# Performance work log

Measured on AMD Instinct MI355X. Metric: run time of the kernel, lower is better.

Reference implementation:

```python
import jax, jax.numpy as jnp
import numpy as np
from jax.scipy.special import gammaln

D_CAT = 20000   # input_dim: number of multinomial categories (tree leaves)
HID = 128       # hidden_dim
BATCH = 128     # batch_size (must match eta's leading dim)
INIT = 1e-3     # init_scale
LOG_SIGMA_SQ0 = 0.01


def _balance_basis(D):
    """Sparse ILR balance basis (D-1, D) from a balanced binary tree.
    Row for an internal node with l left / r right leaves has
    +sqrt(r/(l(l+r))) on left leaves and -sqrt(l/(r(l+r))) on right leaves.
    Mirrors sparse_balance_basis(random_linkage(D)) structurally (rows sum to 0,
    orthonormal), with ~D*log2(D) nonzeros."""
    rows, cols, vals = [], [], []
    stack = [(0, D)]
    r = 0
    while stack:
        lo, hi = stack.pop()
        n = hi - lo
        if n < 2:
            continue
        mid = lo + n // 2
        l, rt = mid - lo, hi - mid
        a = np.sqrt(rt / (l * (l + rt)))
        b = -np.sqrt(l / (rt * (l + rt)))
        cols.extend(range(lo, hi))
        vals.extend([a] * l + [b] * rt)
        rows.extend([r] * n)
        r += 1
        stack.append((lo, mid))
        stack.append((mid, hi))
    assert r == D - 1
    return (np.asarray(rows, np.int32), np.asarray(cols, np.int32),
            np.asarray(vals, np.float32))


def setup_inputs() -> dict:
    key = jax.random.key(0)
    ks = jax.random.split(key, 4)
    rows, cols, vals = _balance_basis(D_CAT)
    x = jax.random.randint(ks[0], (BATCH, D_CAT), 0, 20).astype(jnp.float32)
    enc_w = jax.random.normal(ks[1], (HID, D_CAT - 1), jnp.float32) * INIT   # nn.Linear weight (out,in)
    dec_w = jax.random.normal(ks[2], (D_CAT - 1, HID), jnp.float32) * INIT
    eta = jax.random.normal(ks[3], (BATCH, D_CAT - 1), jnp.float32) * INIT
    return {
        "x": x,
        "psi_rows": jnp.asarray(rows),
        "psi_cols": jnp.asarray(cols),
        "psi_vals": jnp.asarray(vals),
        "enc_w": enc_w,
        "dec_w": dec_w,
        "variational_logvars": jnp.zeros((HID,), jnp.float32),
        "log_sigma_sq": jnp.float32(LOG_SIGMA_SQ0),
        "eta": eta,
    }


def reference(x, psi_rows, psi_cols, psi_vals, enc_w, dec_w,
              variational_logvars, log_sigma_sq, eta):
    B, D = x.shape
    dm1 = D - 1
    k = enc_w.shape[0]

    # ilr(imputer(x), Psi): hx = (Psi @ log(x+1)^T)^T via sparse gather+segment_sum
    lx = jnp.log(x + 1.0)                                  # (B, D)
    contrib = lx[:, psi_cols] * psi_vals                   # (B, nnz)
    hx = jax.ops.segment_sum(contrib.T, psi_rows, num_segments=dm1,
                             indices_are_sorted=True).T    # (B, D-1)

    z_mean = hx @ enc_w.T                                  # (B, k)
    mu = z_mean @ dec_w.T                                  # (B, D-1)

    # prior: standard Normal log-prob of z_mean, mean over all elements
    prior_loss = jnp.mean(-0.5 * z_mean ** 2 - 0.5 * jnp.log(2.0 * jnp.pi))

    # MultivariateNormalFactorIdentity(mu, var, Dv, W): Sigma = var*I + W diag(Dv) W^T
    # Woodbury / matrix-determinant-lemma log-prob of eta.
    var = jnp.exp(log_sigma_sq)
    Dv = jnp.exp(variational_logvars)                      # (k,)
    sD = jnp.sqrt(Dv)
    WtW = dec_w.T @ dec_w                                  # (k, k)
    M = jnp.eye(k, dtype=x.dtype) + (sD[:, None] * WtW * sD[None, :]) / var
    _, logdetM = jnp.linalg.slogdet(M)
    logdet = dm1 * log_sigma_sq + logdetM                  # log|Sigma|
    diff = eta - mu                                        # (B, D-1)
    u = (diff @ dec_w) * sD                                # (B, k)
    Minv_u = jnp.linalg.solve(M, u.T).T                    # (B, k)
    quad = jnp.sum(diff ** 2, -1) / var - jnp.sum(u * Minv_u, -1) / (var ** 2)
    logit_loss = jnp.mean(-0.5 * (dm1 * jnp.log(2.0 * jnp.pi) + logdet + quad))

    # Multinomial log-prob: logits = (Psi^T @ eta^T)^T, sparse scatter over categories
    c2 = eta[:, psi_rows] * psi_vals                       # (B, nnz)
    logits = jax.ops.segment_sum(c2.T, psi_cols, num_segments=D).T  # (B, D)
    logn = jax.nn.log_softmax(logits, axis=-1)
    mult = (gammaln(x.sum(-1) + 1.0) - gammaln(x + 1.0).sum(-1)
            + (x * logn).sum(-1))
    mult_loss = jnp.mean(mult)

    return -(mult_loss + logit_loss + prior_loss)
```

## Files before the change

kernel.cpp:

```cpp
#include <hip/hip_runtime.h>
#include <hip/hip_bf16.h>

#define DD 20000
#define DM1 19999
#define NB 128
#define SCB 625
#define SCH 32
#define KS 128
#define GCH 157
#define CMAX 16

typedef __hip_bfloat16 bf16;
typedef __attribute__((ext_vector_type(8))) short short8v;
typedef __attribute__((ext_vector_type(16))) float f32x16;

__device__ __align__(16) float g_lxT[(size_t)DD * NB];
__device__ __align__(16) float g_etaT[(size_t)DM1 * NB];
__device__ unsigned short g_etaTb[(size_t)DM1 * NB];
__device__ __align__(16) float g_hxT[(size_t)DM1 * NB];
__device__ __align__(16) float g_S[(size_t)(DD + 1) * NB];
__device__ __align__(16) float g_part[SCB * NB];
__device__ __align__(16) float g_p0[SCB * NB];
__device__ __align__(16) float g_p1[SCB * NB];
__device__ __align__(16) float g_p2[SCB * NB];
__device__ __align__(16) float g_pc[(size_t)KS * 49152];
__device__ __align__(16) float g_zT[16384];
__device__ __align__(16) float g_WtW[16384];
__device__ __align__(16) float g_e0[16384];
__device__ float g_S1[NB], g_S2[NB], g_sumx[NB], g_slg[NB], g_quad1[NB], g_q2[NB];
__device__ float g_tr[4];
__device__ int g_f32flag;
__device__ int g_rlo[DM1], g_rmid[DM1], g_rhi[DM1];
__device__ float g_ra[DM1], g_rb[DM1];
__device__ int g_ccnt[DD];
__device__ int g_crow[(size_t)DD * CMAX];
__device__ __align__(16) float g_cval[(size_t)DD * CMAX];

__device__ __constant__ float c_lgf[24] = {
  0.f, 0.f, 0.6931471806f, 1.7917594692f, 3.1780538303f, 4.7874917428f,
  6.5792512120f, 8.5251613611f, 10.6046029027f, 12.8018274801f,
  15.1044125731f, 17.5023078459f, 19.9872144957f, 22.5521638531f,
  25.1912211827f, 27.8992713838f, 30.6718601061f, 33.5050734501f,
  36.3954452081f, 39.3398841872f, 42.3356164608f, 45.3801388985f,
  48.4711813518f, 51.6066755678f};

__device__ __forceinline__ float b2f(bf16 v) { return __bfloat162float(v); }

__device__ __forceinline__ float wave_red_sum(float v) {
#pragma unroll
  for (int off = 32; off > 0; off >>= 1) v += __shfl_down(v, off, 64);
  return v;
}

__device__ __forceinline__ float load_in(const void* src, size_t idx, int f32) {
  return f32 ? ((const float*)src)[idx] : b2f(((const bf16*)src)[idx]);
}

__device__ __forceinline__ int lbound(const int* a, int n, int key) {
  int lo = 0, hi = n;
  while (lo < hi) { int m = (lo + hi) >> 1; if (a[m] < key) lo = m + 1; else hi = m; }
  return lo;
}

__device__ __forceinline__ unsigned short f2bf(float f) {
  unsigned u = __float_as_uint(f);
  unsigned r = (u + 0x7fffu + ((u >> 16) & 1u)) >> 16;
  return (unsigned short)r;
}

__global__ __launch_bounds__(256)
void k_zero(const void* __restrict__ xv) {
  int i = blockIdx.x * 256 + threadIdx.x;
  if (i < DD * CMAX) g_cval[i] = 0.f;
  if (i < DD) g_ccnt[i] = 0;
  if (i < NB) { g_S1[i] = 0.f; g_S2[i] = 0.f; }
  if (i < 4) g_tr[i] = 0.f;
  if (i == 0) {
    const float* xf = (const float*)xv;
    int ok = 1;
    for (int q = 0; q < 64; q++) {
      float v = xf[q];
      if (!(v >= 0.f && v < 20.5f && floorf(v) == v)) { ok = 0; break; }
    }
    g_f32flag = ok;
  }
}

__global__ __launch_bounds__(256)
void k_trans2(const void* __restrict__ xsrc, const void* __restrict__ esrc) {
  __shared__ float tile[32][33];
  int which = blockIdx.x >= SCB;
  int bx = which ? (int)blockIdx.x - SCB : (int)blockIdx.x;
  const int N = which ? DM1 : DD;
  const void* src = which ? esrc : xsrc;
  float* dst = which ? g_etaT : g_lxT;
  int f32 = g_f32flag;
  int c0 = bx * 32, b0 = blockIdx.y * 32;
  int tx = threadIdx.x, ty = threadIdx.y;
  float r0[4] = {}, r1[4] = {}, r2[4] = {};
#pragma unroll
  for (int i = 0; i < 32; i += 8) {
    int c = c0 + tx;
    float v = 0.f, lx = 0.f;
    if (c < N) {
      v = load_in(src, (size_t)(b0 + ty + i) * N + c, f32);
      lx = which ? v : logf(v + 1.0f);
    }
    tile[ty + i][tx] = lx;
    int i4 = i >> 3;
    if (!which) {
      r0[i4] += v;
      int ix = (int)(v + 0.5f);
      r1[i4] += (ix < 24) ? c_lgf[ix] : lgammaf(v + 1.0f);
      r2[i4] += lx;
    } else {
      r0[i4] += v * v;
    }
  }
#pragma unroll
  for (int i4 = 0; i4 < 4; i4++) {
#pragma unroll
    for (int off = 16; off > 0; off >>= 1) {
      r0[i4] += __shfl_down(r0[i4], off, 32);
      r1[i4] += __shfl_down(r1[i4], off, 32);
      r2[i4] += __shfl_down(r2[i4], off, 32);
    }
    if (tx == 0) {
      int b = b0 + ty + i4 * 8;
      size_t o = (size_t)bx * NB + b;
      if (!which) { g_p0[o] = r0[i4]; g_p1[o] = r1[i4]; g_part[o] = r2[i4]; }
      else g_p2[o] = r0[i4];
    }
  }
  __syncthreads();
#pragma unroll
  for (int i = 0; i < 32; i += 8) {
    int c = c0 + ty + i;
    if (c < N) {
      float vv = tile[tx][ty + i];
      dst[(size_t)c * NB + b0 + tx] = vv;
      if (which) g_etaTb[(size_t)c * NB + b0 + tx] = f2bf(vv);
    }
  }
}

__global__ __launch_bounds__(256)
void k_aux(const int* __restrict__ rows, const int* __restrict__ cols,
           const void* __restrict__ vals, int nnz, int nbc, int nbr) {
  int f32 = g_f32flag;
  int bxx = blockIdx.x;
  if (bxx < nbc) {
    int j = bxx * 256 + threadIdx.x;
    if (j >= nnz) return;
    int c = cols[j];
    int slot = atomicAdd(&g_ccnt[c], 1);
    if (slot < CMAX) {
      g_crow[(size_t)c * CMAX + slot] = rows[j];
      g_cval[(size_t)c * CMAX + slot] = load_in(vals, j, f32);
    }
    return;
  }
  if (bxx < nbc + nbr) {
    int r = (bxx - nbc) * 256 + threadIdx.x;
    if (r >= DM1) return;
    int s = lbound(rows, nnz, r), e = lbound(rows, nnz, r + 1);
    int lo = cols[s], hi = cols[e - 1] + 1;
    int lo_i = s, hi_i = e - 1;
    while (hi_i - lo_i > 1) {
      int m = (lo_i + hi_i) >> 1;
      if (load_in(vals, m, f32) < 0.f) hi_i = m; else lo_i = m;
    }
    g_rlo[r] = lo; g_rmid[r] = lo + (hi_i - s); g_rhi[r] = hi;
    g_ra[r] = load_in(vals, s, f32);
    g_rb[r] = load_in(vals, e - 1, f32);
    return;
  }
  __shared__ float sc[256];
  int b = bxx - nbc - nbr;
  int t = threadIdx.x;
  float v[3];
  float s = 0.f;
#pragma unroll
  for (int q = 0; q < 3; q++) {
    int idx = t * 3 + q;
    v[q] = (idx < SCB) ? g_part[(size_t)idx * NB + b] : 0.f;
    s += v[q];
  }
  sc[t] = s;
  __syncthreads();
  for (int d = 1; d < 256; d <<= 1) {
    float add = (t >= d) ? sc[t - d] : 0.f;
    __syncthreads();
    sc[t] += add;
    __syncthreads();
  }
  float run = (t == 0) ? 0.f : sc[t - 1];
#pragma unroll
  for (int q = 0; q < 3; q++) {
    int idx = t * 3 + q;
    if (idx < SCB) {
      float tmp = v[q];
      g_part[(size_t)idx * NB + b] = run;
      run += tmp;
    }
  }
  float s0 = 0.f, s1 = 0.f, s2 = 0.f;
  for (int idx = t; idx < SCB; idx += 256) {
    size_t o = (size_t)idx * NB + b;
    s0 += g_p0[o];
    s1 += g_p1[o];
    s2 += g_p2[o];
  }
  __syncthreads();
  sc[t] = s0;
  __syncthreads();
  for (int d = 128; d > 0; d >>= 1) { if (t < d) sc[t] += sc[t + d]; __syncthreads(); }
  if (t == 0) g_sumx[b] = sc[0];
  __syncthreads();
  sc[t] = s1;
  __syncthreads();
  for (int d = 128; d > 0; d >>= 1) { if (t < d) sc[t] += sc[t + d]; __syncthreads(); }
  if (t == 0) g_slg[b] = sc[0];
  __syncthreads();
  sc[t] = s2;
  __syncthreads();
  for (int d = 128; d > 0; d >>= 1) { if (t < d) sc[t] += sc[t + d]; __syncthreads(); }
  if (t == 0) g_quad1[b] = sc[0];
}

__global__ __launch_bounds__(128)
void k_scanC_S() {
  int j = blockIdx.x, b = threadIdx.x;
  int c0 = j * SCH, c1 = min(c0 + SCH, DD);
  float acc = g_part[j * NB + b];
  for (int c = c0; c < c1; c++) {
    g_S[(size_t)c * NB + b] = acc;
    acc += g_lxT[(size_t)c * NB + b];
  }
  if (c1 == DD && c0 < DD) g_S[(size_t)DD * NB + b] = acc;
}

__global__ __launch_bounds__(512)
void k_hxlg() {
  int t = threadIdx.x;
  if ((int)blockIdx.x < SCB) {
    __shared__ int slo[32], smid[32], shi[32];
    __shared__ float sa[32], sb[32];
    int r0 = blockIdx.x * 32;
    if (t < 32) {
      int r = r0 + t;
      if (r < DM1) {
        slo[t] = g_rlo[r]; smid[t] = g_rmid[r]; shi[t] = g_rhi[r];
        sa[t] = g_ra[r];   sb[t] = g_rb[r];
      }
    }
    __syncthreads();
    int b = t & 127, g = t >> 7;
#pragma unroll
    for (int q = 0; q < 8; q++) {
      int rr = g * 8 + q;
      int r = r0 + rr;
      if (r >= DM1) break;
      float sl = g_S[(size_t)slo[rr]  * NB + b];
      float sm = g_S[(size_t)smid[rr] * NB + b];
      float sh = g_S[(size_t)shi[rr]  * NB + b];
      g_hxT[(size_t)r * NB + b] = sa[rr] * (sm - sl) + sb[rr] * (sh - sm);
    }
    return;
  }
  __shared__ int   sr[32][CMAX];
  __shared__ float sv[32][CMAX];
  __shared__ float s1s[4][128], s2s[4][128];
  int c0 = ((int)blockIdx.x - SCB) * 32;
  {
    int cc = t >> 4, l = t & 15;
    sr[cc][l] = g_crow[(size_t)(c0 + cc) * CMAX + l];
    sv[cc][l] = g_cval[(size_t)(c0 + cc) * CMAX + l];
  }
  __syncthreads();
  int b = t & 127;
  int qg = t >> 7;
  float s1 = 0.f, s2 = 0.f;
#pragma unroll
  for (int q = 0; q < 8; q += 4) {
    int cc = qg * 8 + q;
    unsigned short ev[4][CMAX];
#pragma unroll
    for (int j = 0; j < 4; j++)
#pragma unroll
      for (int l = 0; l < CMAX; l++)
        ev[j][l] = g_etaTb[(size_t)sr[cc + j][l] * NB + b];
    float lxv[4];
#pragma unroll
    for (int j = 0; j < 4; j++)
      lxv[j] = g_lxT[(size_t)(c0 + cc + j) * NB + b];
#pragma unroll
    for (int j = 0; j < 4; j++) {
      float lg = 0.f;
#pragma unroll
      for (int l = 0; l < CMAX; l++)
        lg += sv[cc + j][l] * __uint_as_float((unsigned)ev[j][l] << 16);
      s1 += expf(lg);
      s2 += (expf(lxv[j]) - 1.0f) * lg;
    }
  }
  s1s[qg][b] = s1;
  s2s[qg][b] = s2;
  __syncthreads();
  if (qg == 0) {
    atomicAdd(&g_S1[b], s1s[0][b] + s1s[1][b] + s1s[2][b] + s1s[3][b]);
    atomicAdd(&g_S2[b], s2s[0][b] + s2s[1][b] + s2s[2][b] + s2s[3][b]);
  }
}

__global__ __launch_bounds__(512)
void k_atb3(const void* __restrict__ dec, const void* __restrict__ enc) {
  __shared__ unsigned short Ah[128][40], Al[128][40];
  __shared__ unsigned short Bh[64][40],  Bl[64][40];
  int f32 = g_f32flag;
  int mat = blockIdx.y >> 1;
  int j0 = (blockIdx.y & 1) * 64;
  int ks = blockIdx.x * GCH;
  int ke = min(ks + GCH, DM1);
  int t = threadIdx.x;
  int lane = t & 63;
  int w = t >> 6;
  int wi = (w >> 1) * 32;
  int wj = (w & 1) * 32;
  int ai = t & 127;
  int akg = t >> 7;
  int bj = t & 63;
  int bkg = (t >> 6) & 3;

  f32x16 acc;
#pragma unroll
  for (int r = 0; r < 16; r++) acc[r] = 0.f;

  for (int kb = ks; kb < ke; kb += 32) {
    float av[8];
#pragma unroll
    for (int q = 0; q < 8; q++) {
      int k = kb + akg * 8 + q;
      float v = 0.f;
      if (k < ke) {
        if (mat == 2)      v = g_hxT[(size_t)k * NB + ai];
        else if (mat == 1) v = g_etaT[(size_t)k * NB + ai];
        else               v = load_in(dec, (size_t)k * 128 + ai, f32);
      }
      av[q] = v;
    }
    float bv[8];
    if (t < 256) {
#pragma unroll
      for (int q = 0; q < 8; q++) {
        int k = kb + bkg * 8 + q;
        float v = 0.f;
        if (k < ke) {
          if (mat == 2) v = load_in(enc, (size_t)(j0 + bj) * DM1 + k, f32);
          else          v = load_in(dec, (size_t)k * 128 + j0 + bj, f32);
        }
        bv[q] = v;
      }
    }
    __syncthreads();
    {
      short8v h8, l8;
#pragma unroll
      for (int q = 0; q < 8; q++) {
        unsigned short h = f2bf(av[q]);
        float hf = __uint_as_float((unsigned)h << 16);
        h8[q] = (short)h;
        l8[q] = (short)f2bf(av[q] - hf);
      }
      *(short8v*)&Ah[ai][akg * 8] = h8;
      *(short8v*)&Al[ai][akg * 8] = l8;
    }
    if (t < 256) {
      short8v h8, l8;
#pragma unroll
      for (int q = 0; q < 8; q++) {
        unsigned short h = f2bf(bv[q]);
        float hf = __uint_as_float((unsigned)h << 16);
        h8[q] = (short)h;
        l8[q] = (short)f2bf(bv[q] - hf);
      }
      *(short8v*)&Bh[bj][bkg * 8] = h8;
      *(short8v*)&Bl[bj][bkg * 8] = l8;
    }
    __syncthreads();
#pragma unroll
    for (int s = 0; s < 2; s++) {
      int k0 = s * 16 + (lane >> 5) * 8;
      int ar = wi + (lane & 31);
      int bc = wj + (lane & 31);
      short8v a_h = *(const short8v*)&Ah[ar][k0];
      short8v a_l = *(const short8v*)&Al[ar][k0];
      short8v b_h = *(const short8v*)&Bh[bc][k0];
      short8v b_l = *(const short8v*)&Bl[bc][k0];
      acc = __builtin_amdgcn_mfma_f32_32x32x16_bf16(a_h, b_h, acc, 0, 0, 0);
      acc = __builtin_amdgcn_mfma_f32_32x32x16_bf16(a_l, b_h, acc, 0, 0, 0);
      acc = __builtin_amdgcn_mfma_f32_32x32x16_bf16(a_h, b_l, acc, 0, 0, 0);
    }
  }
  float* dst = g_pc + (size_t)blockIdx.x * 49152 + mat * 16384;
  int col = j0 + wj + (lane & 31);
#pragma unroll
  for (int r = 0; r < 16; r++) {
    int row = wi + (r & 3) + 8 * (r >> 2) + 4 * (lane >> 5);
    dst[row * 128 + col] = acc[r];
  }
}

__global__ __launch_bounds__(256)
void k_red3() {
  __shared__ float sh[256];
  int t = threadIdx.x;
  int e = blockIdx.x * 64 + (t & 63);
  int sg = t >> 6;
  float acc = 0.f;
#pragma unroll 8
  for (int s = sg * 32; s < sg * 32 + 32; s++)
    acc += g_pc[(size_t)s * 49152 + e];
  sh[t] = acc;
  __syncthreads();
  if (t < 64) {
    float v = sh[t] + sh[t + 64] + sh[t + 128] + sh[t + 192];
    int g = blockIdx.x * 64 + t;
    int m = g >> 14, e2 = g & 16383;
    if (m == 0) g_WtW[e2] = v;
    else if (m == 1) g_e0[e2] = v;
    else g_zT[(e2 & 127) * 128 + (e2 >> 7)] = v;
  }
}

__global__ __launch_bounds__(128)
void k_pu(const void* __restrict__ logvars, const void* __restrict__ lsq) {
  __shared__ float sh0[128], sh1[128], sh2[128], sh3[128], sh4[128], sh5[128];
  __shared__ float sds[128];
  int j = threadIdx.x;
  int f32 = g_f32flag;
  float invvar = expf(-load_in(lsq, 0, f32));
  sds[j] = expf(0.5f * load_in(logvars, j, f32));
  __syncthreads();
  if ((int)blockIdx.x < 128) {
    int i = blockIdx.x;
    float sdj = sds[j];
    float p = sds[i] * sdj * g_WtW[i * 128 + j] * invvar;
    sh0[j] = p;
    __syncthreads();
    float acc = 0.f;
    for (int k = 0; k < 128; k++)
      acc += sh0[k] * (sds[k] * sdj * g_WtW[k * 128 + j] * invvar);
    float v1 = wave_red_sum((i == j) ? p : 0.f);
    float v2 = wave_red_sum(p * p);
    float v3 = wave_red_sum(p * acc);
    float v4 = wave_red_sum(acc * acc);
    if ((j & 63) == 0) {
      atomicAdd(&g_tr[0], v1);
      atomicAdd(&g_tr[1], v2);
      atomicAdd(&g_tr[2], v3);
      atomicAdd(&g_tr[3], v4);
    }
  } else {
    int b = blockIdx.x - 128, k = j;
    float sdk = sds[k];
    sh0[k] = g_zT[(size_t)k * 128 + b];
    __syncthreads();
    float e0k = g_e0[b * 128 + k];
    float zWk = 0.f;
    for (int m = 0; m < 128; m++) zWk += sh0[m] * g_WtW[m * 128 + k];
    float u = (e0k - zWk) * sdk;
    sh1[k] = u;
    sh5[k] = sh0[k] * (zWk - 2.f * e0k);
    __syncthreads();
    float v1 = 0.f;
    for (int m = 0; m < 128; m++) v1 += sds[m] * g_WtW[m * 128 + k] * sh1[m];
    v1 *= sdk * invvar;
    sh2[k] = v1;
    __syncthreads();
    float v2 = 0.f;
    for (int m = 0; m < 128; m++) v2 += sds[m] * g_WtW[m * 128 + k] * sh2[m];
    v2 *= sdk * invvar;
    sh3[k] = v2;
    __syncthreads();
    float v3 = 0.f;
    for (int m = 0; m < 128; m++) v3 += sds[m] * g_WtW[m * 128 + k] * sh3[m];
    v3 *= sdk * invvar;
    sh4[k] = u * (u - v1 + v2 - v3);
    __syncthreads();
    for (int s = 64; s > 0; s >>= 1) {
      if (k < s) { sh4[k] += sh4[k + s]; sh5[k] += sh5[k + s]; }
      __syncthreads();
    }
    if (k == 0) {
      g_q2[b] = sh4[0];
      g_quad1[b] += sh5[0];
    }
  }
}

__global__ __launch_bounds__(128)
void k_final(const void* __restrict__ lsq, float* __restrict__ out) {
  __shared__ double red[128];
  __shared__ float redz[128];
  int b = threadIdx.x;
  int f32 = g_f32flag;
  float zs = 0.f;
  for (int i = b; i < 16384; i += 128) { float v = g_zT[i]; zs += v * v; }
  redz[b] = zs;
  const double LOG2PI = 1.837877066409345483560659472811;
  float lsqv = load_in(lsq, 0, f32);
  double var = exp((double)lsqv);
  double lse = log((double)g_S1[b]);
  double sumx = (double)g_sumx[b];
  double t1 = lgamma(sumx + 1.0) - (double)g_slg[b];
  double mult_b = t1 + (double)g_S2[b] - sumx * lse;
  double logdetM = (double)g_tr[0] - 0.5 * (double)g_tr[1]
                 + (1.0 / 3.0) * (double)g_tr[2] - 0.25 * (double)g_tr[3];
  double logdet = (double)DM1 * (double)lsqv + logdetM;
  double quad_b = (double)g_quad1[b] / var - (double)g_q2[b] / (var * var);
  double logit_b = -0.5 * ((double)DM1 * LOG2PI + logdet + quad_b);
  red[b] = mult_b + logit_b;
  __syncthreads();
  for (int s = 64; s > 0; s >>= 1) {
    if (b < s) { red[b] += red[b + s]; redz[b] += redz[b + s]; }
    __syncthreads();
  }
  if (b == 0) {
    double ml = red[0] / 128.0;
    double prior = -0.5 * (double)redz[0] / 16384.0 - 0.5 * LOG2PI;
    out[0] = (float)(-(ml + prior));
  }
}

extern "C" void kernel_launch(void* const* d_in, const int* in_sizes, int n_in,
                              void* d_out, int out_size, void* d_ws, size_t ws_size,
                              hipStream_t stream) {
  const void* x     = d_in[0];
  const int*  rows  = (const int*)d_in[1];
  const int*  cols  = (const int*)d_in[2];
  const void* vals  = d_in[3];
  const void* enc_w = d_in[4];
  const void* dec_w = d_in[5];
  const void* lvars = d_in[6];
  const void* lsq   = d_in[7];
  const void* eta   = d_in[8];
  float* out = (float*)d_out;
  int nnz = in_sizes[1];
  (void)d_ws; (void)ws_size;

  int nbc = (nnz + 255) / 256;
  int nbr = (DM1 + 255) / 256;

  k_zero<<<(DD * CMAX + 255) / 256, 256, 0, stream>>>(x);
  k_trans2<<<dim3(2 * SCB, 4), dim3(32, 8), 0, stream>>>(x, eta);
  k_aux<<<nbc + nbr + 128, 256, 0, stream>>>(rows, cols, vals, nnz, nbc, nbr);
  k_scanC_S<<<SCB, 128, 0, stream>>>();
  k_hxlg<<<2 * SCB, 512, 0, stream>>>();
  k_atb3<<<dim3(KS, 6), 512, 0, stream>>>(dec_w, enc_w);
  k_red3<<<768, 256, 0, stream>>>();
  k_pu<<<256, 128, 0, stream>>>(lvars, lsq);
  k_final<<<1, 128, 0, stream>>>(lsq, out);
}
```

Measured before the change: 245.0 us.

## Fuse zero kernel into transpose, parallelize scan, interleave hxlg blocks, widen red3

Folds the zero-init kernel into k_trans2 as extra blocks, with each transpose block re-probing the input dtype itself instead of reading the flag, which saves one launch. k_scanC_S now uses 512 threads, splitting each 32-column chunk into four 8-column groups that are combined through shared memory, so the serial dependent chain is shorter. k_hxlg interleaves its two block types (even and odd block ids) so both run together. k_red3 spreads the reduction over twice as many blocks with shorter per-thread loops. The cost is redundant dtype-probe reads in every transpose block.

```diff
diff --git a/kernel.cpp b/kernel.cpp
--- a/kernel.cpp
+++ b/kernel.cpp
@@ -68,33 +68,35 @@
   return (unsigned short)r;
 }
 
-__global__ __launch_bounds__(256)
-void k_zero(const void* __restrict__ xv) {
-  int i = blockIdx.x * 256 + threadIdx.x;
-  if (i < DD * CMAX) g_cval[i] = 0.f;
-  if (i < DD) g_ccnt[i] = 0;
-  if (i < NB) { g_S1[i] = 0.f; g_S2[i] = 0.f; }
-  if (i < 4) g_tr[i] = 0.f;
-  if (i == 0) {
-    const float* xf = (const float*)xv;
-    int ok = 1;
-    for (int q = 0; q < 64; q++) {
-      float v = xf[q];
-      if (!(v >= 0.f && v < 20.5f && floorf(v) == v)) { ok = 0; break; }
-    }
-    g_f32flag = ok;
-  }
+__device__ __forceinline__ int probe_f32(const void* xv) {
+  const float* xf = (const float*)xv;
+  int ok = 1;
+  for (int q = 0; q < 64; q++) {
+    float v = xf[q];
+    if (!(v >= 0.f && v < 20.5f && floorf(v) == v)) { ok = 0; break; }
+  }
+  return ok;
 }
 
 __global__ __launch_bounds__(256)
 void k_trans2(const void* __restrict__ xsrc, const void* __restrict__ esrc) {
+  if ((int)blockIdx.x >= 2 * SCB) {
+    int i = (((int)blockIdx.x - 2 * SCB) * 4 + (int)blockIdx.y) * 256
+            + (int)threadIdx.x + (int)threadIdx.y * 32;
+    if (i < DD * CMAX) g_cval[i] = 0.f;
+    if (i < DD) g_ccnt[i] = 0;
+    if (i < NB) { g_S1[i] = 0.f; g_S2[i] = 0.f; }
+    if (i < 4) g_tr[i] = 0.f;
+    if (i == 0) g_f32flag = probe_f32(xsrc);
+    return;
+  }
   __shared__ float tile[32][33];
   int which = blockIdx.x >= SCB;
   int bx = which ? (int)blockIdx.x - SCB : (int)blockIdx.x;
   const int N = which ? DM1 : DD;
   const void* src = which ? esrc : xsrc;
   float* dst = which ? g_etaT : g_lxT;
-  int f32 = g_f32flag;
+  int f32 = probe_f32(xsrc);
   int c0 = bx * 32, b0 = blockIdx.y * 32;
   int tx = threadIdx.x, ty = threadIdx.y;
   float r0[4] = {}, r1[4] = {}, r2[4] = {};
@@ -228,25 +230,40 @@
   if (t == 0) g_quad1[b] = sc[0];
 }
 
-__global__ __launch_bounds__(128)
+__global__ __launch_bounds__(512)
 void k_scanC_S() {
-  int j = blockIdx.x, b = threadIdx.x;
-  int c0 = j * SCH, c1 = min(c0 + SCH, DD);
-  float acc = g_part[j * NB + b];
-  for (int c = c0; c < c1; c++) {
-    g_S[(size_t)c * NB + b] = acc;
-    acc += g_lxT[(size_t)c * NB + b];
-  }
-  if (c1 == DD && c0 < DD) g_S[(size_t)DD * NB + b] = acc;
+  __shared__ float ksum[4][128];
+  int j = blockIdx.x;
+  int t = threadIdx.x;
+  int b = t & 127, kg = t >> 7;
+  int c0 = j * SCH + kg * 8;
+  float lv[8];
+#pragma unroll
+  for (int q = 0; q < 8; q++)
+    lv[q] = g_lxT[(size_t)(c0 + q) * NB + b];
+  float lsum = 0.f;
+#pragma unroll
+  for (int q = 0; q < 8; q++) lsum += lv[q];
+  ksum[kg][b] = lsum;
+  __syncthreads();
+  float base = g_part[(size_t)j * NB + b];
+  for (int g = 0; g < kg; g++) base += ksum[g][b];
+#pragma unroll
+  for (int q = 0; q < 8; q++) {
+    g_S[(size_t)(c0 + q) * NB + b] = base;
+    base += lv[q];
+  }
+  if (j == SCB - 1 && kg == 3) g_S[(size_t)DD * NB + b] = base;
 }
 
 __global__ __launch_bounds__(512)
 void k_hxlg() {
   int t = threadIdx.x;
-  if ((int)blockIdx.x < SCB) {
+  int bid = (int)blockIdx.x >> 1;
+  if (((int)blockIdx.x & 1) == 0) {
     __shared__ int slo[32], smid[32], shi[32];
     __shared__ float sa[32], sb[32];
-    int r0 = blockIdx.x * 32;
+    int r0 = bid * 32;
     if (t < 32) {
       int r = r0 + t;
       if (r < DM1) {
@@ -271,7 +288,7 @@
   __shared__ int   sr[32][CMAX];
   __shared__ float sv[32][CMAX];
   __shared__ float s1s[4][128], s2s[4][128];
-  int c0 = ((int)blockIdx.x - SCB) * 32;
+  int c0 = bid * 32;
   {
     int cc = t >> 4, l = t & 15;
     sr[cc][l] = g_crow[(size_t)(c0 + cc) * CMAX + l];
@@ -415,18 +432,20 @@
 void k_red3() {
   __shared__ float sh[256];
   int t = threadIdx.x;
-  int e = blockIdx.x * 64 + (t & 63);
-  int sg = t >> 6;
+  int e = blockIdx.x * 32 + (t & 31);
+  int sg = t >> 5;
   float acc = 0.f;
-#pragma unroll 8
-  for (int s = sg * 32; s < sg * 32 + 32; s++)
+#pragma unroll 16
+  for (int s = sg * 16; s < sg * 16 + 16; s++)
     acc += g_pc[(size_t)s * 49152 + e];
   sh[t] = acc;
   __syncthreads();
-  if (t < 64) {
-    float v = sh[t] + sh[t + 64] + sh[t + 128] + sh[t + 192];
-    int g = blockIdx.x * 64 + t;
-    int m = g >> 14, e2 = g & 16383;
+  if (t < 32) {
+    float v = 0.f;
+#pragma unroll
+    for (int g = 0; g < 8; g++) v += sh[t + g * 32];
+    int gg = blockIdx.x * 32 + t;
+    int m = gg >> 14, e2 = gg & 16383;
     if (m == 0) g_WtW[e2] = v;
     else if (m == 1) g_e0[e2] = v;
     else g_zT[(e2 & 127) * 128 + (e2 >> 7)] = v;
@@ -551,14 +570,14 @@
 
   int nbc = (nnz + 255) / 256;
   int nbr = (DM1 + 255) / 256;
-
-  k_zero<<<(DD * CMAX + 255) / 256, 256, 0, stream>>>(x);
-  k_trans2<<<dim3(2 * SCB, 4), dim3(32, 8), 0, stream>>>(x, eta);
+  int zb = (DD * CMAX + 1023) / 1024;
+
+  k_trans2<<<dim3(2 * SCB + zb, 4), dim3(32, 8), 0, stream>>>(x, eta);
   k_aux<<<nbc + nbr + 128, 256, 0, stream>>>(rows, cols, vals, nnz, nbc, nbr);
-  k_scanC_S<<<SCB, 128, 0, stream>>>();
+  k_scanC_S<<<SCB, 512, 0, stream>>>();
   k_hxlg<<<2 * SCB, 512, 0, stream>>>();
   k_atb3<<<dim3(KS, 6), 512, 0, stream>>>(dec_w, enc_w);
-  k_red3<<<768, 256, 0, stream>>>();
+  k_red3<<<1536, 256, 0, stream>>>();
   k_pu<<<256, 128, 0, stream>>>(lvars, lsq);
   k_final<<<1, 128, 0, stream>>>(lsq, out);
 }
```

Result: no change. 248.5 us (+1.4%).
